# Kernel tuning notes

Hardware: AMD Instinct MI355X
Metric: run time of the kernel (lower is better)

The kernel has to match this reference:

```python
import jax, jax.numpy as jnp
import numpy as np

E = 524288
IN = 256
OUT = 256
T = 16


def setup_inputs() -> dict:
    key = jax.random.key(0)
    k1, k2, k3 = jax.random.split(key, 3)
    x_j = jax.random.normal(k1, (E, IN), dtype=jnp.float32)
    # kaiming-uniform-ish init for the per-type weights
    bound = 1.0 / np.sqrt(IN)
    rel_weights = jax.random.uniform(k2, (T, IN, OUT), dtype=jnp.float32,
                                     minval=-bound, maxval=bound)
    edge_types = jax.random.randint(k3, (E,), 0, T, dtype=jnp.int64)
    return {"x_j": x_j, "rel_weights": rel_weights, "edge_types": edge_types}


def reference(x_j, rel_weights, edge_types):
    # Faithful to the torch semantics:
    #   out[i] = x_j[edge_types[i]] @ rel_weights[edge_types[i]]
    # (the torch code's broadcasted matmul + [i, edge_types[i]] gather reduces
    #  to a per-type matvec followed by an index gather).
    num_types = rel_weights.shape[0]
    # y[t] = x_j[t] @ W[t], shape [T, OUT] -- tiny compute
    y = jnp.einsum('ti,tio->to', x_j[:num_types], rel_weights)
    # memory-bound gather to [E, OUT]
    return y[edge_types]
```

## Files before the change

### kernel.cpp

```cpp
#include <hip/hip_runtime.h>


#define RL_IN  256
#define RL_OUT 256
#define RL_T   16

typedef float f32x4 __attribute__((ext_vector_type(4)));

__global__ __launch_bounds__(1024)
void rl_compute_y(const float* __restrict__ x,
                  const float* __restrict__ W,
                  float* __restrict__ y) {
    const int t = blockIdx.x;
    const int c = threadIdx.x >> 8;
    const int o = threadIdx.x & 255;
    const int i0 = c * 64;

    __shared__ float xs[RL_IN];
    if (threadIdx.x < RL_IN) xs[threadIdx.x] = x[t * RL_IN + threadIdx.x];
    __syncthreads();

    const float* Wt = W + (size_t)t * RL_IN * RL_OUT + (size_t)i0 * RL_OUT;
    float acc = 0.0f;
#pragma unroll 8
    for (int i = 0; i < 64; ++i) {
        acc += xs[i0 + i] * Wt[i * RL_OUT + o];
    }

    __shared__ float part[4][RL_OUT];
    part[c][o] = acc;
    __syncthreads();
    if (c == 0) {
        y[t * RL_OUT + o] = part[0][o] + part[1][o] + part[2][o] + part[3][o];
    }
}

#define SPAN 512

__global__ __launch_bounds__(256)
void rl_gather(const int* __restrict__ et,
               const f32x4* __restrict__ y4,
               f32x4* __restrict__ out4,
               int E) {
    __shared__ f32x4 ys[RL_T * (RL_OUT / 4)];
    __shared__ int tys[4][SPAN];

    for (int i = threadIdx.x; i < RL_T * (RL_OUT / 4); i += blockDim.x)
        ys[i] = y4[i];

    const int lane = threadIdx.x & 63;
    const int w    = threadIdx.x >> 6;
    const int gw   = blockIdx.x * 4 + w;
    const int nW   = gridDim.x * 4;

    __syncthreads();

    const int4* et4 = (const int4*)et;

    for (long base = (long)gw * SPAN; base < E; base += (long)nW * SPAN) {
        if (base + SPAN <= E) {
            int4* t4 = (int4*)tys[w];
            t4[lane]      = et4[base / 4 + lane];
            t4[64 + lane] = et4[base / 4 + 64 + lane];
            size_t o0 = (size_t)base * 64 + lane;
#pragma unroll 8
            for (int r = 0; r < SPAN; ++r) {
                const int t = tys[w][r];
                out4[o0 + (size_t)r * 64] = ys[t * 64 + lane];
            }
        } else {
            for (long row = base; row < E; ++row) {
                const int t = et[row];
                out4[(size_t)row * 64 + lane] = ys[t * 64 + lane];
            }
        }
    }
}

extern "C" void kernel_launch(void* const* d_in, const int* in_sizes, int n_in,
                              void* d_out, int out_size, void* d_ws, size_t ws_size,
                              hipStream_t stream) {
    const float* x_j  = (const float*)d_in[0];
    const float* W    = (const float*)d_in[1];
    const int*   et   = (const int*)d_in[2];
    float*       out  = (float*)d_out;

    const int E = in_sizes[2];

    float* y = (float*)d_ws;

    rl_compute_y<<<RL_T, 1024, 0, stream>>>(x_j, W, y);

    rl_gather<<<256, 256, 0, stream>>>(et, (const f32x4*)y,
                                       (f32x4*)out, E);
}
```

Before: 113.9 us.

## Interleave gather work across waves with nontemporal stores and larger grid

The gather kernel now hands out groups of four rows to waves in an interleaved order instead of contiguous 512-row spans. Edge types are staged sixteen int4 groups at a time in shared memory. Output writes use nontemporal stores, and the grid grows from 256 to 2048 blocks to raise occupancy and memory-level parallelism for the 512 MB write stream. It also drops the tail path, so it assumes E is divisible by 4. There is no barrier between the lane<16 shared-memory write and the reads by the whole wave; this relies on wave-synchronous execution.

```diff
diff --git a/kernel.cpp b/kernel.cpp
--- a/kernel.cpp
+++ b/kernel.cpp
@@ -35,15 +35,13 @@
     }
 }
 
-#define SPAN 512
-
 __global__ __launch_bounds__(256)
 void rl_gather(const int* __restrict__ et,
                const f32x4* __restrict__ y4,
                f32x4* __restrict__ out4,
                int E) {
     __shared__ f32x4 ys[RL_T * (RL_OUT / 4)];
-    __shared__ int tys[4][SPAN];
+    __shared__ int4  tys[4][16];
 
     for (int i = threadIdx.x; i < RL_T * (RL_OUT / 4); i += blockDim.x)
         ys[i] = y4[i];
@@ -52,27 +50,30 @@
     const int w    = threadIdx.x >> 6;
     const int gw   = blockIdx.x * 4 + w;
     const int nW   = gridDim.x * 4;
+    const int G    = E >> 2;
+    const int4* et4 = (const int4*)et;
 
     __syncthreads();
 
-    const int4* et4 = (const int4*)et;
-
-    for (long base = (long)gw * SPAN; base < E; base += (long)nW * SPAN) {
-        if (base + SPAN <= E) {
-            int4* t4 = (int4*)tys[w];
-            t4[lane]      = et4[base / 4 + lane];
-            t4[64 + lane] = et4[base / 4 + 64 + lane];
-            size_t o0 = (size_t)base * 64 + lane;
-#pragma unroll 8
-            for (int r = 0; r < SPAN; ++r) {
-                const int t = tys[w][r];
-                out4[o0 + (size_t)r * 64] = ys[t * 64 + lane];
-            }
-        } else {
-            for (long row = base; row < E; ++row) {
-                const int t = et[row];
-                out4[(size_t)row * 64 + lane] = ys[t * 64 + lane];
-            }
+    for (int j0 = 0; j0 * nW + gw < G; j0 += 16) {
+        if (lane < 16) {
+            const int g = gw + (j0 + lane) * nW;
+            tys[w][lane] = (g < G) ? et4[g] : make_int4(0, 0, 0, 0);
+        }
+#pragma unroll
+        for (int s = 0; s < 16; ++s) {
+            const int g = gw + (j0 + s) * nW;
+            if (g >= G) break;
+            const int4 tv = tys[w][s];
+            const size_t r0 = (size_t)g * 4;
+            f32x4 v0 = ys[tv.x * 64 + lane];
+            f32x4 v1 = ys[tv.y * 64 + lane];
+            f32x4 v2 = ys[tv.z * 64 + lane];
+            f32x4 v3 = ys[tv.w * 64 + lane];
+            __builtin_nontemporal_store(v0, &out4[(r0 + 0) * 64 + lane]);
+            __builtin_nontemporal_store(v1, &out4[(r0 + 1) * 64 + lane]);
+            __builtin_nontemporal_store(v2, &out4[(r0 + 2) * 64 + lane]);
+            __builtin_nontemporal_store(v3, &out4[(r0 + 3) * 64 + lane]);
         }
     }
 }
@@ -91,6 +92,6 @@
 
     rl_compute_y<<<RL_T, 1024, 0, stream>>>(x_j, W, y);
 
-    rl_gather<<<256, 256, 0, stream>>>(et, (const f32x4*)y,
-                                       (f32x4*)out, E);
+    rl_gather<<<2048, 256, 0, stream>>>(et, (const f32x4*)y,
+                                        (f32x4*)out, E);
 }
```

Measured after the change: 115.4 us. No clear change (+1.2%).
